# Kernel optimization log

Measured on AMD Instinct MI355X. Metric: run time of the kernel, lower is better.

Reference implementation:

```python
import jax, jax.numpy as jnp
import numpy as np

DIM = 128; MOTION = 128; HEADS = 8; WS = 8; B2 = 4; H = 192; W = 192; HID = 512

def _ln(x, w, b, eps=1e-5):
    m = x.mean(-1, keepdims=True)
    v = ((x - m) ** 2).mean(-1, keepdims=True)
    return (x - m) / jnp.sqrt(v + eps) * w + b

def _win_part(x, ws):
    B, Hh, Ww, C = x.shape
    x = x.reshape(B, Hh // ws, ws, Ww // ws, ws, C).transpose(0, 1, 3, 2, 4, 5)
    return x.reshape(-1, ws * ws, C)

def _win_rev(win, ws, Hh, Ww):
    nwB, N, C = win.shape
    B = nwB // ((Hh // ws) * (Ww // ws))
    x = win.reshape(B, Hh // ws, Ww // ws, ws, ws, C).transpose(0, 1, 3, 2, 4, 5)
    return x.reshape(B, Hh, Ww, C)

def setup_inputs() -> dict:
    key = jax.random.key(0)
    ks = jax.random.split(key, 12)
    def lin(k, o, i):
        return jax.random.normal(k, (o, i), jnp.float32) * 0.02
    return {
        "x": jax.random.normal(ks[0], (B2, H * W, DIM), jnp.float32),
        "cor": jax.random.uniform(ks[1], (B2, H * W, 2), dtype=jnp.float32),
        "q_w": lin(ks[2], DIM, DIM),
        "kv_w": lin(ks[3], 2 * DIM, DIM),
        "cor_w": lin(ks[4], MOTION, 2),
        "proj_w": lin(ks[5], DIM, DIM), "proj_b": jnp.zeros((DIM,), jnp.float32),
        "mproj_w": lin(ks[6], MOTION, MOTION), "mproj_b": jnp.zeros((MOTION,), jnp.float32),
        "norm1_w": jnp.ones((DIM,), jnp.float32), "norm1_b": jnp.zeros((DIM,), jnp.float32),
        "norm2_w": jnp.ones((DIM,), jnp.float32), "norm2_b": jnp.zeros((DIM,), jnp.float32),
        "fc1_w": lin(ks[7], HID, DIM), "fc1_b": jnp.zeros((HID,), jnp.float32),
        "dw_w": jax.random.normal(ks[8], (HID, 1, 3, 3), jnp.float32) * 0.1,
        "dw_b": jnp.zeros((HID,), jnp.float32),
        "fc2_w": lin(ks[9], DIM, HID), "fc2_b": jnp.zeros((DIM,), jnp.float32),
    }

def _attn(x1, x2, cor, q_w, kv_w, cor_w, proj_w, proj_b, mproj_w, mproj_b):
    # x1,x2: (nwB, N, C) windowed query / cross-frame key-value; cor: (nwB, N, 2)
    B, N, C = x1.shape
    hd = C // HEADS
    mh = MOTION // HEADS
    scale = hd ** -0.5
    q = (x1 @ q_w.T).reshape(B, N, HEADS, hd).transpose(0, 2, 1, 3)
    kv = (x2 @ kv_w.T).reshape(B, N, 2, HEADS, hd).transpose(2, 0, 3, 1, 4)
    k, v = kv[0], kv[1]
    ce = cor @ cor_w.T                                   # (B, N, MOTION)
    ceh = ce.reshape(B, N, HEADS, mh).transpose(0, 2, 1, 3)
    attn = jax.nn.softmax(jnp.einsum('bhnd,bhmd->bhnm', q, k) * scale, axis=-1)
    xo = jnp.einsum('bhnm,bhmd->bhnd', attn, v).transpose(0, 2, 1, 3).reshape(B, N, C)
    crev = jnp.einsum('bhnm,bhmd->bhnd', attn, ceh).transpose(0, 2, 1, 3).reshape(B, N, MOTION)
    motion = (crev - ce) @ mproj_w.T + mproj_b
    return xo @ proj_w.T + proj_b, motion

def _mlp(x, fc1_w, fc1_b, dw_w, dw_b, fc2_w, fc2_b):
    B, N, _ = x.shape
    h = x @ fc1_w.T + fc1_b                              # (B, N, HID)
    hm = h.transpose(0, 2, 1).reshape(B, HID, H, W)
    hm = jax.lax.conv_general_dilated(hm, dw_w, (1, 1), 'SAME',
                                      feature_group_count=HID,
                                      dimension_numbers=('NCHW', 'OIHW', 'NCHW'))
    hm = hm + dw_b[None, :, None, None]
    h = jax.nn.gelu(hm.reshape(B, HID, N).transpose(0, 2, 1), approximate=False)
    return h @ fc2_w.T + fc2_b

def reference(x, cor, q_w, kv_w, cor_w, proj_w, proj_b, mproj_w, mproj_b,
              norm1_w, norm1_b, norm2_w, norm2_b, fc1_w, fc1_b, dw_w, dw_b, fc2_w, fc2_b):
    shortcut = x
    xn = _ln(x, norm1_w, norm1_b).reshape(B2, H, W, DIM)
    cm = cor.reshape(B2, H, W, 2)
    xw = _win_part(xn, WS)                               # (nwB, 64, DIM)
    cw = _win_part(cm, WS)
    nwB = xw.shape[0]
    xr = jnp.concatenate([xw[nwB // 2:], xw[:nwB // 2]], axis=0)
    xa, xm = _attn(xw, xr, cw, q_w, kv_w, cor_w, proj_w, proj_b, mproj_w, mproj_b)
    xa = _win_rev(xa, WS, H, W).reshape(B2, H * W, DIM)
    xm = _win_rev(xm, WS, H, W).reshape(B2, H * W, MOTION)
    x = shortcut + xa
    x = x + _mlp(_ln(x, norm2_w, norm2_b), fc1_w, fc1_b, dw_w, dw_b, fc2_w, fc2_b)
    return x, xm
```

## Files before the change

### kernel.cpp

```cpp
#include <hip/hip_runtime.h>
#include <hip/hip_bf16.h>
#include <math.h>

#define NB 4
#define IMG 192
#define HW (IMG*IMG)
#define T_TOT (NB*HW)
#define HID 512
#define NWB 2304
#define WPB 576
#define NWS 24

typedef __bf16 bf16;
typedef __bf16 bf8 __attribute__((ext_vector_type(8)));
typedef __bf16 bf4 __attribute__((ext_vector_type(4)));
typedef float f32x4 __attribute__((ext_vector_type(4)));

#define MFMA(a,b,c) __builtin_amdgcn_mfma_f32_16x16x32_bf16(a,b,c,0,0,0)

#define BAR_LGKM asm volatile("s_waitcnt lgkmcnt(0)\ns_barrier" ::: "memory")
#define BAR_ALL  asm volatile("s_waitcnt vmcnt(0) lgkmcnt(0)\ns_barrier" ::: "memory")

__device__ __forceinline__ int swz128(int row, int col){ return row*128 + (col ^ ((row&7)<<3)); }

__device__ __forceinline__ bf8 zero_bf8(){
  bf8 z = { (bf16)0.f,(bf16)0.f,(bf16)0.f,(bf16)0.f,(bf16)0.f,(bf16)0.f,(bf16)0.f,(bf16)0.f };
  return z;
}
__device__ __forceinline__ f32x4 zero_f4(){ f32x4 z = {0.f,0.f,0.f,0.f}; return z; }

typedef const __attribute__((address_space(1))) unsigned int as1_u32;
typedef __attribute__((address_space(3))) unsigned int as3_u32;
__device__ __forceinline__ void gload16(const bf16* g, bf16* l){
  __builtin_amdgcn_global_load_lds((as1_u32*)g, (as3_u32*)l, 16, 0, 0);
}

__global__ void k_cvt(const float* __restrict__ s, bf16* __restrict__ d, int n, float scale){
  int i = blockIdx.x*256 + threadIdx.x;
  if (i < n) d[i] = (bf16)(s[i]*scale);
}

__global__ void k_a2(const float* __restrict__ mproj_w, const float* __restrict__ cor_w,
                     bf16* __restrict__ a2w){
  int idx = blockIdx.x*256 + threadIdx.x;
  if (idx >= 4096) return;
  int o = idx >> 5, k = idx & 31;
  float acc = 0.f;
  if (k < 16){
    int h = k >> 1, c = k & 1;
    #pragma unroll
    for (int i=0;i<16;i++)
      acc += mproj_w[o*128 + h*16 + i] * cor_w[(h*16+i)*2 + c];
  }
  a2w[o*32 + k] = (bf16)acc;
}

__global__ __launch_bounds__(256) void k_ln1(
    const float* __restrict__ x, const float* __restrict__ cor,
    const float* __restrict__ n1w, const float* __restrict__ n1b,
    bf16* __restrict__ xn, bf16* __restrict__ cwb)
{
  int tid = threadIdx.x, wm = tid>>6, l = tid&63;
  int lr = l & 15, tg = l >> 4;
  int t = blockIdx.x*16 + wm*4 + tg;

  const float* xp = x + (size_t)t*128 + lr*8;
  float4 a = *(const float4*)xp;
  float4 b4 = *(const float4*)(xp+4);
  float s  = a.x+a.y+a.z+a.w + b4.x+b4.y+b4.z+b4.w;
  float sq = a.x*a.x+a.y*a.y+a.z*a.z+a.w*a.w + b4.x*b4.x+b4.y*b4.y+b4.z*b4.z+b4.w*b4.w;
  #pragma unroll
  for (int m=1;m<16;m<<=1){ s += __shfl_xor(s,m,16); sq += __shfl_xor(sq,m,16); }
  float mean = s * (1.0f/128.0f);
  float var  = sq * (1.0f/128.0f) - mean*mean;
  float rstd = rsqrtf(var + 1e-5f);

  float4 nw0 = *(const float4*)(n1w + lr*8), nw1 = *(const float4*)(n1w + lr*8 + 4);
  float4 nb0 = *(const float4*)(n1b + lr*8), nb1 = *(const float4*)(n1b + lr*8 + 4);

  bf8 o;
  o[0] = (bf16)((a.x -mean)*rstd*nw0.x + nb0.x);
  o[1] = (bf16)((a.y -mean)*rstd*nw0.y + nb0.y);
  o[2] = (bf16)((a.z -mean)*rstd*nw0.z + nb0.z);
  o[3] = (bf16)((a.w -mean)*rstd*nw0.w + nb0.w);
  o[4] = (bf16)((b4.x-mean)*rstd*nw1.x + nb1.x);
  o[5] = (bf16)((b4.y-mean)*rstd*nw1.y + nb1.y);
  o[6] = (bf16)((b4.z-mean)*rstd*nw1.z + nb1.z);
  o[7] = (bf16)((b4.w-mean)*rstd*nw1.w + nb1.w);

  int b = t / HW, r = t % HW;
  int yy = r / IMG, xx = r % IMG;
  int win = b*WPB + (yy>>3)*NWS + (xx>>3);
  int n = ((yy&7)<<3) + (xx&7);
  *(bf8*)(xn + (size_t)win*8192 + n*128 + lr*8) = o;

  if (lr < 2) cwb[(size_t)win*128 + n*2 + lr] = (bf16)cor[(size_t)t*2 + lr];
}

__global__ __launch_bounds__(256) void k_attn(
    const bf16* __restrict__ xn, const bf16* __restrict__ cw,
    const bf16* __restrict__ wq, const bf16* __restrict__ wkv,
    const bf16* __restrict__ wpj, const bf16* __restrict__ a2w,
    const float* __restrict__ proj_b, const float* __restrict__ mproj_b,
    const float* __restrict__ x_in, float* __restrict__ x1, float* __restrict__ out_m)
{
  __shared__ __align__(16) bf16 s_s [64*128];
  __shared__ __align__(16) bf16 s_k [64*128];
  __shared__ __align__(16) bf16 s_vT[128*64];
  __shared__ __align__(16) bf16 s_P [2][64*64];
  __shared__ __align__(16) bf16 s_cT[16*64];
  __shared__ __align__(16) bf16 s_D [64*32];

  int tid = threadIdx.x, wm = tid>>6, l = tid&63;
  int lr = l & 15, lg = l >> 4;
  int win = blockIdx.x;
  int partner = (win + NWB/2) % NWB;
  const bf16* xw_g = xn + (size_t)win*8192;
  const bf16* xr_g = xn + (size_t)partner*8192;

  bf8 xrv[4], xwv[4];
  #pragma unroll
  for (int tci=0;tci<4;tci++){
    int chunk = tid + tci*256;
    int row = chunk>>4, c0 = (chunk&15)*8;
    xrv[tci] = *(const bf8*)(xr_g + row*128 + c0);
    xwv[tci] = *(const bf8*)(xw_g + row*128 + c0);
  }
  bf16 cwv = (bf16)0.f;
  if (tid < 128) cwv = cw[(size_t)win*128 + tid];

  *(unsigned long long*)&s_cT[tid*4] = 0ull;
  *(unsigned long long*)&s_D[tid*8]   = 0ull;
  *(unsigned long long*)&s_D[tid*8+4] = 0ull;
  #pragma unroll
  for (int tci=0;tci<4;tci++){
    int chunk = tid + tci*256;
    int row = chunk>>4, c0 = (chunk&15)*8;
    *(bf8*)&s_s[swz128(row,c0)] = xrv[tci];
  }
  BAR_LGKM;

  if (tid < 128){
    int c = tid & 1, m = tid >> 1;
    s_cT[c*64 + (m ^ (c<<3))] = cwv;
  } else if (tid < 192){
    int m = tid - 128;
    s_cT[2*64 + (m ^ 16)] = (bf16)1.0f;
  }
  {
    bf8 af[4];
    #pragma unroll
    for (int ks=0;ks<4;ks++) af[ks] = *(const bf8*)&s_s[swz128(wm*16+lr, ks*32 + lg*8)];
    #pragma unroll
    for (int nt=0;nt<8;nt++){
      f32x4 acc = zero_f4();
      #pragma unroll
      for (int ks=0;ks<4;ks++){
        bf8 bfr = *(const bf8*)(wkv + (nt*16+lr)*128 + ks*32 + lg*8);
        acc = MFMA(af[ks], bfr, acc);
      }
      #pragma unroll
      for (int j=0;j<4;j++){
        int row = wm*16 + lg*4 + j;
        s_k[swz128(row, nt*16+lr)] = (bf16)acc[j];
      }
    }
    #pragma unroll
    for (int nt=0;nt<8;nt++){
      f32x4 acc = zero_f4();
      #pragma unroll
      for (int ks=0;ks<4;ks++){
        bf8 bfr = *(const bf8*)(wkv + (128 + nt*16+lr)*128 + ks*32 + lg*8);
        acc = MFMA(af[ks], bfr, acc);
      }
      #pragma unroll
      for (int j=0;j<4;j++){
        int tok = wm*16 + lg*4 + j;
        int chc = nt*16 + lr;
        s_vT[chc*64 + (tok ^ ((chc&7)<<3))] = (bf16)acc[j];
      }
    }
  }
  BAR_LGKM;

  #pragma unroll
  for (int tci=0;tci<4;tci++){
    int chunk = tid + tci*256;
    int row = chunk>>4, c0 = (chunk&15)*8;
    *(bf8*)&s_s[swz128(row,c0)] = xwv[tci];
  }
  BAR_LGKM;

  {
    bf8 af[4];
    #pragma unroll
    for (int ks=0;ks<4;ks++) af[ks] = *(const bf8*)&s_s[swz128(wm*16+lr, ks*32 + lg*8)];
    #pragma unroll
    for (int nt=0;nt<8;nt++){
      f32x4 acc = zero_f4();
      #pragma unroll
      for (int ks=0;ks<4;ks++){
        bf8 bfr = *(const bf8*)(wq + (nt*16+lr)*128 + ks*32 + lg*8);
        acc = MFMA(af[ks], bfr, acc);
      }
      #pragma unroll
      for (int j=0;j<4;j++){
        int row = wm*16 + lg*4 + j;
        s_s[swz128(row, nt*16+lr)] = (bf16)acc[j];
      }
    }
  }

  float mycw[4] = {0.f,0.f,0.f,0.f};
  if (lr < 2){
    #pragma unroll
    for (int j=0;j<4;j++){
      int row = wm*16 + lg*4 + j;
      mycw[j] = (float)s_cT[lr*64 + (row ^ (lr<<3))];
    }
  }

  #pragma unroll
  for (int h=0;h<8;h++){
    bf8 aS = zero_bf8();
    if (l < 32) aS = *(const bf8*)&s_s[swz128(wm*16+lr, h*16 + lg*8)];
    f32x4 accS[4];
    #pragma unroll
    for (int nt=0;nt<4;nt++){
      bf8 bSv = zero_bf8();
      if (l < 32) bSv = *(const bf8*)&s_k[swz128(nt*16+lr, h*16 + lg*8)];
      accS[nt] = MFMA(aS, bSv, zero_f4());
    }
    bf16* Pb = &s_P[h&1][0];
    #pragma unroll
    for (int nt=0;nt<4;nt++){
      #pragma unroll
      for (int j=0;j<4;j++){
        int row = wm*16 + lg*4 + j;
        Pb[row*64 + ((nt*16+lr) ^ ((row&7)<<3))] = (bf16)__expf(accS[nt][j]);
      }
    }
    f32x4 accO = zero_f4(), accPC = zero_f4();
    #pragma unroll
    for (int ks=0;ks<2;ks++){
      int rowA = wm*16 + lr;
      bf8 aP = *(const bf8*)&Pb[rowA*64 + ((ks*32 + lg*8) ^ ((rowA&7)<<3))];
      int chc = h*16 + lr;
      bf8 bV = *(const bf8*)&s_vT[chc*64 + ((ks*32 + lg*8) ^ ((chc&7)<<3))];
      accO = MFMA(aP, bV, accO);
      bf8 bC = *(const bf8*)&s_cT[lr*64 + ((ks*32 + lg*8) ^ ((lr&7)<<3))];
      accPC = MFMA(aP, bC, accPC);
    }
    #pragma unroll
    for (int j=0;j<4;j++){
      int row = wm*16 + lg*4 + j;
      float rs = __shfl(accPC[j], (l & 48) + 2, 64);
      float inv = __builtin_amdgcn_rcpf(rs);
      s_s[swz128(row, h*16+lr)] = (bf16)(accO[j]*inv);
      if (lr < 2)
        s_D[row*32 + ((2*h+lr) ^ ((row&3)<<3))] = (bf16)(accPC[j]*inv - mycw[j]);
    }
  }

  int b  = win / WPB, wi = win % WPB;
  int wy = wi / NWS,  wx = wi % NWS;
  {
    bf8 af[4];
    #pragma unroll
    for (int ks=0;ks<4;ks++) af[ks] = *(const bf8*)&s_s[swz128(wm*16+lr, ks*32 + lg*8)];
    #pragma unroll
    for (int nt=0;nt<8;nt++){
      f32x4 acc = zero_f4();
      #pragma unroll
      for (int ks=0;ks<4;ks++){
        bf8 bfr = *(const bf8*)(wpj + (nt*16+lr)*128 + ks*32 + lg*8);
        acc = MFMA(af[ks], bfr, acc);
      }
      int col = nt*16 + lr;
      float pb = proj_b[col];
      #pragma unroll
      for (int j=0;j<4;j++){
        int tok = wm*16 + lg*4 + j;
        int yy = wy*8 + (tok>>3), xx = wx*8 + (tok&7);
        size_t addr = ((size_t)b*HW + yy*IMG + xx)*128 + col;
        x1[addr] = acc[j] + pb + x_in[addr];
      }
    }
  }
  {
    int rowA = wm*16 + lr;
    bf8 afD = *(const bf8*)&s_D[rowA*32 + ((lg*8) ^ ((rowA&3)<<3))];
    #pragma unroll
    for (int nt=0;nt<8;nt++){
      bf8 bfr = *(const bf8*)(a2w + (nt*16+lr)*32 + lg*8);
      f32x4 acc = MFMA(afD, bfr, zero_f4());
      int col = nt*16 + lr;
      float pb = mproj_b[col];
      #pragma unroll
      for (int j=0;j<4;j++){
        int tok = wm*16 + lg*4 + j;
        int yy = wy*8 + (tok>>3), xx = wx*8 + (tok&7);
        size_t addr = ((size_t)b*HW + yy*IMG + xx)*128 + col;
        out_m[addr] = acc[j] + pb;
      }
    }
  }
}

__global__ __launch_bounds__(256) void k_fc1(
    const float* __restrict__ x1, const float* __restrict__ n2w, const float* __restrict__ n2b,
    const bf16* __restrict__ wf1, const float* __restrict__ fc1b, bf16* __restrict__ h)
{
  __shared__ __align__(16) bf16 s_a[64*128];
  int tid = threadIdx.x, wm = tid>>6, l = tid&63;
  int lr = l & 15, lg = l >> 4;
  size_t t0 = (size_t)blockIdx.x * 64;

  float4 nw0 = *(const float4*)(n2w + lr*8), nw1 = *(const float4*)(n2w + lr*8 + 4);
  float4 nb0 = *(const float4*)(n2b + lr*8), nb1 = *(const float4*)(n2b + lr*8 + 4);

  #pragma unroll
  for (int rr=0; rr<4; rr++){
    int row = wm*16 + rr*4 + lg;
    const float* xp = x1 + (t0+row)*128 + lr*8;
    float4 a = *(const float4*)xp;
    float4 b4 = *(const float4*)(xp+4);
    float s  = a.x+a.y+a.z+a.w + b4.x+b4.y+b4.z+b4.w;
    float sq = a.x*a.x+a.y*a.y+a.z*a.z+a.w*a.w + b4.x*b4.x+b4.y*b4.y+b4.z*b4.z+b4.w*b4.w;
    #pragma unroll
    for (int m=1;m<16;m<<=1){ s += __shfl_xor(s,m,16); sq += __shfl_xor(sq,m,16); }
    float mean = s*(1.f/128.f), var = sq*(1.f/128.f) - mean*mean;
    float rstd = rsqrtf(var + 1e-5f);
    bf8 o;
    o[0] = (bf16)((a.x -mean)*rstd*nw0.x + nb0.x);
    o[1] = (bf16)((a.y -mean)*rstd*nw0.y + nb0.y);
    o[2] = (bf16)((a.z -mean)*rstd*nw0.z + nb0.z);
    o[3] = (bf16)((a.w -mean)*rstd*nw0.w + nb0.w);
    o[4] = (bf16)((b4.x-mean)*rstd*nw1.x + nb1.x);
    o[5] = (bf16)((b4.y-mean)*rstd*nw1.y + nb1.y);
    o[6] = (bf16)((b4.z-mean)*rstd*nw1.z + nb1.z);
    o[7] = (bf16)((b4.w-mean)*rstd*nw1.w + nb1.w);
    *(bf8*)&s_a[swz128(row, lr*8)] = o;
  }
  __syncthreads();

  bf8 af[4];
  #pragma unroll
  for (int ks=0;ks<4;ks++) af[ks] = *(const bf8*)&s_a[swz128(wm*16+lr, ks*32 + lg*8)];
  for (int ntb=0; ntb<4; ntb++){
    f32x4 acc[8];
    #pragma unroll
    for (int q8=0;q8<8;q8++){
      acc[q8] = zero_f4();
      #pragma unroll
      for (int ks=0;ks<4;ks++){
        int ocol = ntb*128 + q8*16 + lr;
        bf8 bfr = *(const bf8*)(wf1 + (size_t)ocol*128 + ks*32 + lg*8);
        acc[q8] = MFMA(af[ks], bfr, acc[q8]);
      }
    }
    #pragma unroll
    for (int q8=0;q8<8;q8++){
      int col = ntb*128 + q8*16 + lr;
      float bb = fc1b[col];
      #pragma unroll
      for (int j=0;j<4;j++){
        int tl = wm*16 + lg*4 + j;
        h[(t0+tl)*512 + col] = (bf16)(acc[q8][j] + bb);
      }
    }
  }
}

__global__ __launch_bounds__(256) void k_mlp2(
    const bf16* __restrict__ h, const float* __restrict__ dww, const float* __restrict__ dwb,
    const bf16* __restrict__ wf2, const float* __restrict__ fc2b,
    const float* __restrict__ x1, float* __restrict__ outx)
{
  __shared__ __align__(16) bf16 s_hh[2][100*128];
  int tid = threadIdx.x, wm = tid>>6, l = tid&63;
  int lr = l & 15, lg = l >> 4;
  int tile = 575 - blockIdx.x, b = 3 - blockIdx.y;
  int ty = tile / 24, tx = tile % 24;
  int cq = (tid & 31) * 4;
  int tg2 = tid >> 5;

  f32x4 acc[8];
  #pragma unroll
  for (int q=0;q<8;q++) acc[q] = zero_f4();

  bool edge = (ty==0) | (ty==23) | (tx==0) | (tx==23);
  if (edge){
    #pragma unroll
    for (int it=0; it<7; it++){
      int idx = it*256 + tid;
      if (idx < 1600){
        int pos = idx>>4, c0 = (idx&15)*8;
        int hy = pos/10, hx = pos%10;
        int yy = ty*8 + hy - 1, xx = tx*8 + hx - 1;
        if (yy<0 || yy>=IMG || xx<0 || xx>=IMG){
          *(bf8*)&s_hh[0][pos*128 + c0] = zero_bf8();
          *(bf8*)&s_hh[1][pos*128 + c0] = zero_bf8();
        }
      }
    }
  }

  #define STAGE_DMA(KC, BUF)                                                  \
    _Pragma("unroll")                                                         \
    for (int it=0; it<7; it++){                                               \
      int idx = it*256 + tid;                                                 \
      if (idx < 1600){                                                        \
        int pos = idx>>4, c0 = (idx&15)*8;                                    \
        int hy = pos/10, hx = pos%10;                                         \
        int yy = ty*8 + hy - 1, xx = tx*8 + hx - 1;                           \
        bf16* lb = &s_hh[BUF][it*2048 + wm*512];       \
        if (yy>=0 && yy<IMG && xx>=0 && xx<IMG)                               \
          gload16(h + ((size_t)b*HW + yy*IMG + xx)*512 + (KC)*128 + c0, lb);  \
      }                                                                       \
    }

  STAGE_DMA(0, 0);
  BAR_ALL;

  int cur = 0;
  for (int kc=0;kc<4;kc++){
    if (kc < 3) STAGE_DMA(kc+1, cur^1);

    int chg0 = kc*128 + cq;
    float4 bias4 = *(const float4*)(dwb + chg0);
    float cr[8][4];
    #pragma unroll
    for (int i=0;i<8;i++){ cr[i][0]=bias4.x; cr[i][1]=bias4.y; cr[i][2]=bias4.z; cr[i][3]=bias4.w; }
    #pragma unroll
    for (int dy=0;dy<3;dy++){
      float rv[10][4];
      #pragma unroll
      for (int p=0;p<10;p++){
        bf4 pv = *(const bf4*)&s_hh[cur][((tg2+dy)*10 + p)*128 + cq];
        rv[p][0]=(float)pv[0]; rv[p][1]=(float)pv[1];
        rv[p][2]=(float)pv[2]; rv[p][3]=(float)pv[3];
      }
      #pragma unroll
      for (int dx=0;dx<3;dx++){
        int tq = dy*3+dx;
        float w0 = dww[(chg0+0)*9 + tq];
        float w1 = dww[(chg0+1)*9 + tq];
        float w2 = dww[(chg0+2)*9 + tq];
        float w3 = dww[(chg0+3)*9 + tq];
        #pragma unroll
        for (int i=0;i<8;i++){
          cr[i][0] += rv[i+dx][0]*w0;
          cr[i][1] += rv[i+dx][1]*w1;
          cr[i][2] += rv[i+dx][2]*w2;
          cr[i][3] += rv[i+dx][3]*w3;
        }
      }
    }
    bf4 gout[8];
    #pragma unroll
    for (int i=0;i<8;i++){
      #pragma unroll
      for (int c=0;c<4;c++){
        float hv = cr[i][c];
        float hv2 = hv*hv;
        float v = hv * fmaf(hv2, -0.0713548353f, -1.5957691216f);
        float g = hv * __builtin_amdgcn_rcpf(1.0f + __expf(v));
        gout[i][c] = (bf16)g;
      }
    }
    BAR_LGKM;
    #pragma unroll
    for (int i=0;i<8;i++){
      int pos = (tg2+1)*10 + (i+1);
      *(bf4*)&s_hh[cur][pos*128 + (cq ^ (i<<3))] = gout[i];
    }
    {
      bf8 af[4];
      #pragma unroll
      for (int ks=0;ks<4;ks++){
        int tok = wm*16 + lr;
        int pos = ((tok>>3)+1)*10 + (tok&7) + 1;
        af[ks] = *(const bf8*)&s_hh[cur][pos*128 + ((ks*32 + lg*8) ^ ((lr&7)<<3))];
      }
      #pragma unroll
      for (int q=0;q<8;q++){
        #pragma unroll
        for (int ks=0;ks<4;ks++){
          bf8 bfr = *(const bf8*)(wf2 + (size_t)(q*16+lr)*512 + kc*128 + ks*32 + lg*8);
          acc[q] = MFMA(af[ks], bfr, acc[q]);
        }
      }
    }
    BAR_ALL;
    cur ^= 1;
  }
  #pragma unroll
  for (int q=0;q<8;q++){
    int col = q*16 + lr;
    float bb = fc2b[col];
    #pragma unroll
    for (int j=0;j<4;j++){
      int tok = wm*16 + lg*4 + j;
      int yy = ty*8 + (tok>>3), xx = tx*8 + (tok&7);
      size_t addr = ((size_t)b*HW + yy*IMG + xx)*128 + col;
      outx[addr] = acc[q][j] + bb + x1[addr];
    }
  }
  #undef STAGE_DMA
}

extern "C" void kernel_launch(void* const* d_in, const int* in_sizes, int n_in,
                              void* d_out, int out_size, void* d_ws, size_t ws_size,
                              hipStream_t stream)
{
  const float* x      = (const float*)d_in[0];
  const float* cor    = (const float*)d_in[1];
  const float* q_w    = (const float*)d_in[2];
  const float* kv_w   = (const float*)d_in[3];
  const float* cor_w  = (const float*)d_in[4];
  const float* proj_w = (const float*)d_in[5];
  const float* proj_b = (const float*)d_in[6];
  const float* mproj_w= (const float*)d_in[7];
  const float* mproj_b= (const float*)d_in[8];
  const float* n1w    = (const float*)d_in[9];
  const float* n1b    = (const float*)d_in[10];
  const float* n2w    = (const float*)d_in[11];
  const float* n2b    = (const float*)d_in[12];
  const float* fc1w   = (const float*)d_in[13];
  const float* fc1b   = (const float*)d_in[14];
  const float* dww    = (const float*)d_in[15];
  const float* dwb    = (const float*)d_in[16];
  const float* fc2w   = (const float*)d_in[17];
  const float* fc2b   = (const float*)d_in[18];
  float* out = (float*)d_out;

  char* ws = (char*)d_ws;
  bf16* wq   = (bf16*)(ws + 0);
  bf16* wkv  = (bf16*)(ws + 32768);
  bf16* wpj  = (bf16*)(ws + 98304);
  bf16* a2w  = (bf16*)(ws + 131072);
  bf16* wf1  = (bf16*)(ws + 139264);
  bf16* wf2  = (bf16*)(ws + 270336);
  bf16* xn   = (bf16*)(ws + 401408);
  bf16* cwb  = (bf16*)(ws + 38150144);
  float* x1  = (float*)(ws + 38739968);
  bf16* hbuf = (bf16*)(ws + 114237440);

  k_cvt<<<64,  256, 0, stream>>>(q_w,   wq,  16384, 0.25f);
  k_cvt<<<128, 256, 0, stream>>>(kv_w,  wkv, 32768, 1.0f);
  k_cvt<<<64,  256, 0, stream>>>(proj_w,wpj, 16384, 1.0f);
  k_cvt<<<256, 256, 0, stream>>>(fc1w,  wf1, 65536, 1.0f);
  k_cvt<<<256, 256, 0, stream>>>(fc2w,  wf2, 65536, 1.0f);
  k_a2 <<<16,  256, 0, stream>>>(mproj_w, cor_w, a2w);

  k_ln1 <<<T_TOT/16, 256, 0, stream>>>(x, cor, n1w, n1b, xn, cwb);
  k_attn<<<NWB,      256, 0, stream>>>(xn, cwb, wq, wkv, wpj, a2w, proj_b, mproj_b,
                                       x, x1, out + (size_t)T_TOT*128);
  k_fc1 <<<T_TOT/64, 256, 0, stream>>>(x1, n2w, n2b, wf1, fc1b, hbuf);
  k_mlp2<<<dim3(576,4), 256, 0, stream>>>(hbuf, dww, dwb, wf2, fc2b, x1, out);
}
```

Measured before the change: 539.4 us.

## Merge weight-prep kernels and software-pipeline per-head QK MFMA in attention

Folds the five weight conversion launches and the motion-weight fusion into a single prep kernel, removing five kernel launches. In the attention kernel, the QK^T MFMAs for head h+1 are issued right after head h's exponentiated scores are written to shared memory, so their latency overlaps the PV and motion MFMAs. The score buffer in shared memory drops from double to single buffering. Each wave reads back only its own 16 rows of that buffer, so reuse across heads relies on wave-local ordering.

```diff
diff --git a/kernel.cpp b/kernel.cpp
--- a/kernel.cpp
+++ b/kernel.cpp
@@ -35,14 +35,25 @@
   __builtin_amdgcn_global_load_lds((as1_u32*)g, (as3_u32*)l, 16, 0, 0);
 }
 
-__global__ void k_cvt(const float* __restrict__ s, bf16* __restrict__ d, int n, float scale){
-  int i = blockIdx.x*256 + threadIdx.x;
-  if (i < n) d[i] = (bf16)(s[i]*scale);
-}
-
-__global__ void k_a2(const float* __restrict__ mproj_w, const float* __restrict__ cor_w,
-                     bf16* __restrict__ a2w){
+__global__ __launch_bounds__(256) void k_prep(
+    const float* __restrict__ q_w, const float* __restrict__ kv_w,
+    const float* __restrict__ proj_w, const float* __restrict__ fc1w,
+    const float* __restrict__ fc2w, const float* __restrict__ mproj_w,
+    const float* __restrict__ cor_w,
+    bf16* __restrict__ wq, bf16* __restrict__ wkv, bf16* __restrict__ wpj,
+    bf16* __restrict__ wf1, bf16* __restrict__ wf2, bf16* __restrict__ a2w)
+{
   int idx = blockIdx.x*256 + threadIdx.x;
+  if (idx < 16384){ wq[idx] = (bf16)(q_w[idx]*0.25f); return; }
+  idx -= 16384;
+  if (idx < 32768){ wkv[idx] = (bf16)kv_w[idx]; return; }
+  idx -= 32768;
+  if (idx < 16384){ wpj[idx] = (bf16)proj_w[idx]; return; }
+  idx -= 16384;
+  if (idx < 65536){ wf1[idx] = (bf16)fc1w[idx]; return; }
+  idx -= 65536;
+  if (idx < 65536){ wf2[idx] = (bf16)fc2w[idx]; return; }
+  idx -= 65536;
   if (idx >= 4096) return;
   int o = idx >> 5, k = idx & 31;
   float acc = 0.f;
@@ -107,7 +118,7 @@
   __shared__ __align__(16) bf16 s_s [64*128];
   __shared__ __align__(16) bf16 s_k [64*128];
   __shared__ __align__(16) bf16 s_vT[128*64];
-  __shared__ __align__(16) bf16 s_P [2][64*64];
+  __shared__ __align__(16) bf16 s_P [64*64];
   __shared__ __align__(16) bf16 s_cT[16*64];
   __shared__ __align__(16) bf16 s_D [64*32];
 
@@ -220,31 +231,42 @@
     }
   }
 
-  #pragma unroll
-  for (int h=0;h<8;h++){
+  f32x4 accS[4];
+  {
     bf8 aS = zero_bf8();
-    if (l < 32) aS = *(const bf8*)&s_s[swz128(wm*16+lr, h*16 + lg*8)];
-    f32x4 accS[4];
+    if (l < 32) aS = *(const bf8*)&s_s[swz128(wm*16+lr, lg*8)];
     #pragma unroll
     for (int nt=0;nt<4;nt++){
       bf8 bSv = zero_bf8();
-      if (l < 32) bSv = *(const bf8*)&s_k[swz128(nt*16+lr, h*16 + lg*8)];
+      if (l < 32) bSv = *(const bf8*)&s_k[swz128(nt*16+lr, lg*8)];
       accS[nt] = MFMA(aS, bSv, zero_f4());
     }
-    bf16* Pb = &s_P[h&1][0];
+  }
+  #pragma unroll
+  for (int h=0;h<8;h++){
     #pragma unroll
     for (int nt=0;nt<4;nt++){
       #pragma unroll
       for (int j=0;j<4;j++){
         int row = wm*16 + lg*4 + j;
-        Pb[row*64 + ((nt*16+lr) ^ ((row&7)<<3))] = (bf16)__expf(accS[nt][j]);
+        s_P[row*64 + ((nt*16+lr) ^ ((row&7)<<3))] = (bf16)__expf(accS[nt][j]);
+      }
+    }
+    if (h < 7){
+      bf8 aS = zero_bf8();
+      if (l < 32) aS = *(const bf8*)&s_s[swz128(wm*16+lr, (h+1)*16 + lg*8)];
+      #pragma unroll
+      for (int nt=0;nt<4;nt++){
+        bf8 bSv = zero_bf8();
+        if (l < 32) bSv = *(const bf8*)&s_k[swz128(nt*16+lr, (h+1)*16 + lg*8)];
+        accS[nt] = MFMA(aS, bSv, zero_f4());
       }
     }
     f32x4 accO = zero_f4(), accPC = zero_f4();
     #pragma unroll
     for (int ks=0;ks<2;ks++){
       int rowA = wm*16 + lr;
-      bf8 aP = *(const bf8*)&Pb[rowA*64 + ((ks*32 + lg*8) ^ ((rowA&7)<<3))];
+      bf8 aP = *(const bf8*)&s_P[rowA*64 + ((ks*32 + lg*8) ^ ((rowA&7)<<3))];
       int chc = h*16 + lr;
       bf8 bV = *(const bf8*)&s_vT[chc*64 + ((ks*32 + lg*8) ^ ((chc&7)<<3))];
       accO = MFMA(aP, bV, accO);
@@ -547,12 +569,8 @@
   float* x1  = (float*)(ws + 38739968);
   bf16* hbuf = (bf16*)(ws + 114237440);
 
-  k_cvt<<<64,  256, 0, stream>>>(q_w,   wq,  16384, 0.25f);
-  k_cvt<<<128, 256, 0, stream>>>(kv_w,  wkv, 32768, 1.0f);
-  k_cvt<<<64,  256, 0, stream>>>(proj_w,wpj, 16384, 1.0f);
-  k_cvt<<<256, 256, 0, stream>>>(fc1w,  wf1, 65536, 1.0f);
-  k_cvt<<<256, 256, 0, stream>>>(fc2w,  wf2, 65536, 1.0f);
-  k_a2 <<<16,  256, 0, stream>>>(mproj_w, cor_w, a2w);
+  k_prep<<<784, 256, 0, stream>>>(q_w, kv_w, proj_w, fc1w, fc2w, mproj_w, cor_w,
+                                  wq, wkv, wpj, wf1, wf2, a2w);
 
   k_ln1 <<<T_TOT/16, 256, 0, stream>>>(x, cor, n1w, n1b, xn, cwb);
   k_attn<<<NWB,      256, 0, stream>>>(xn, cwb, wq, wkv, wpj, a2w, proj_b, mproj_b,
```

Result: no change. 531.2 us (-1.5%).
